# Performance work log

Hardware: AMD Instinct MI355X
Metric: run time of the kernel (lower is better)

Reference implementation:

```python
import jax, jax.numpy as jnp
import numpy as np

N_NODES = 100000
N_EDGES = 1600000
IN_DIM = 128      # 1 (degree) + 127 (raw feat)
HID = 128
N_GRAPHS = 100


def setup_inputs() -> dict:
    key = jax.random.key(0)
    ks = jax.random.split(key, 16)
    feat = jax.random.normal(ks[0], (N_NODES, IN_DIM - 1), dtype=jnp.float32)
    src = jax.random.randint(ks[1], (N_EDGES,), 0, N_NODES, dtype=jnp.int32)
    dst = jax.random.randint(ks[2], (N_EDGES,), 0, N_NODES, dtype=jnp.int32)
    graph_ids = jnp.sort(jax.random.randint(ks[3], (N_NODES,), 0, N_GRAPHS, dtype=jnp.int32))
    s = 1.0 / np.sqrt(IN_DIM)
    W0 = jax.random.uniform(ks[4], (HID, IN_DIM), jnp.float32, -s, s)
    b0 = jax.random.uniform(ks[5], (HID,), jnp.float32, -s, s)
    s = 1.0 / np.sqrt(HID)
    W1 = jax.random.uniform(ks[6], (HID, HID), jnp.float32, -s, s)
    b1 = jax.random.uniform(ks[7], (HID,), jnp.float32, -s, s)
    W2 = jax.random.uniform(ks[8], (HID, HID), jnp.float32, -s, s)
    b2 = jax.random.uniform(ks[9], (HID,), jnp.float32, -s, s)
    Wc1 = jax.random.uniform(ks[10], (HID, HID), jnp.float32, -s, s)
    bc1 = jax.random.uniform(ks[11], (HID,), jnp.float32, -s, s)
    Wc2 = jax.random.uniform(ks[12], (1, HID), jnp.float32, -s, s)
    bc2 = jax.random.uniform(ks[13], (1,), jnp.float32, -s, s)
    return {"feat": feat, "src": src, "dst": dst, "graph_ids": graph_ids,
            "num_graphs": N_GRAPHS,
            "W0": W0, "b0": b0, "W1": W1, "b1": b1, "W2": W2, "b2": b2,
            "Wc1": Wc1, "bc1": bc1, "Wc2": Wc2, "bc2": bc2}


def _gcn_layer(h, src, dst, deg, W, b):
    # mean over in-neighbor messages; zero-in-degree nodes keep old h (DGL reduce never fires)
    n = h.shape[0]
    summed = jax.ops.segment_sum(h[src], dst, num_segments=n)  # [N, d]
    mean = summed / jnp.maximum(deg, 1.0)[:, None]
    agg = jnp.where((deg > 0)[:, None], mean, h)
    return jax.nn.relu(agg @ W.T + b)


def reference(feat, src, dst, graph_ids, num_graphs,
              W0, b0, W1, b1, W2, b2, Wc1, bc1, Wc2, bc2):
    n = feat.shape[0]
    deg = jax.ops.segment_sum(jnp.ones(src.shape[0], jnp.float32), dst, num_segments=n)  # in-degrees
    h = jnp.concatenate([deg[:, None], feat], axis=-1)  # [N, IN_DIM]
    for W, b in ((W0, b0), (W1, b1), (W2, b2)):
        h = _gcn_layer(h, src, dst, deg, W, b)
    # dgl.mean_nodes: per-graph mean of node features
    counts = jax.ops.segment_sum(jnp.ones(n, jnp.float32), graph_ids, num_segments=num_graphs)
    hg = jax.ops.segment_sum(h, graph_ids, num_segments=num_graphs) / jnp.maximum(counts, 1.0)[:, None]
    # faithful: classify1 applied twice, no activation (F.relu was passed as bias flag)
    hg = hg @ Wc1.T + bc1
    hg = hg @ Wc1.T + bc1
    hg = hg @ Wc2.T + bc2
    return hg  # [num_graphs, 1]
```

## Files before the change

### kernel.cpp

```cpp
#include <hip/hip_runtime.h>
#include <hip/hip_bf16.h>

#define HID 128
#define NRAW 127
#define BSH 8
#define BNODES 256


typedef __attribute__((ext_vector_type(8))) short short8;
typedef __attribute__((ext_vector_type(4))) float floatx4;
typedef __attribute__((ext_vector_type(2))) float floatx2;

__device__ inline unsigned pack_bf2(float x, float y) {
    unsigned bx = __float_as_uint(x);
    unsigned by = __float_as_uint(y);
    bx += 0x7fffu + ((bx >> 16) & 1u);
    by += 0x7fffu + ((by >> 16) & 1u);
    return (bx >> 16) | (by & 0xffff0000u);
}
__device__ inline float bf_lo(unsigned u) { return __uint_as_float(u << 16); }
__device__ inline float bf_hi(unsigned u) { return __uint_as_float(u & 0xffff0000u); }


__global__ void init_kernel(const float* __restrict__ W0, const float* __restrict__ W1,
                            const float* __restrict__ W2, const float* __restrict__ Wc1,
                            unsigned* __restrict__ O0, unsigned* __restrict__ O1,
                            unsigned* __restrict__ O2, float* __restrict__ Wc1p,
                            int* __restrict__ gbucket, float* __restrict__ hg,
                            float* __restrict__ counts, int G) {
    int id = blockIdx.x * blockDim.x + threadIdx.x;
    if (id < 512) gbucket[id] = 0;
    if (id < G * HID) hg[id] = 0.f;
    if (id < G) counts[id] = 0.f;
    if (id < 16384) {
        int t = id >> 7, p = id & 127;
        Wc1p[id] = Wc1[t * 128 + ((p & 7) * 16 + (p >> 3))];
    }
    if (id < 3 * 8192) {
        int sel = id >> 13, l = id & 8191;
        const float* W = sel == 0 ? W0 : (sel == 1 ? W1 : W2);
        unsigned* O = sel == 0 ? O0 : (sel == 1 ? O1 : O2);
        int o = l >> 6, pp = (l & 63) * 2;
        int k0 = (pp & 7) * 16 + (pp >> 3);
        int k1 = ((pp + 1) & 7) * 16 + ((pp + 1) >> 3);
        O[l] = pack_bf2(W[o * 128 + k0], W[o * 128 + k1]);
    }
}


__global__ __launch_bounds__(256) void bucket_count_kernel(const int* __restrict__ dst,
                                                           int* __restrict__ gbucket,
                                                           int E, int NB) {
    __shared__ int hist[512];
    int t = threadIdx.x;
    for (int b = t; b < NB; b += 256) hist[b] = 0;
    __syncthreads();
    int base = blockIdx.x * 4096;
    #pragma unroll
    for (int j = 0; j < 16; ++j) {
        int e = base + j * 256 + t;
        if (e < E) atomicAdd(&hist[dst[e] >> BSH], 1);
    }
    __syncthreads();
    for (int b = t; b < NB; b += 256) {
        int v = hist[b];
        if (v) atomicAdd(&gbucket[b], v);
    }
}

__global__ void bucket_scan_kernel(const int* __restrict__ gbucket, int* __restrict__ bstart,
                                   int* __restrict__ gcur, int NB, int E) {
    __shared__ int sm[512];
    int t = threadIdx.x;
    int v = (t < NB) ? gbucket[t] : 0;
    sm[t] = v;
    __syncthreads();
    for (int off = 1; off < 512; off <<= 1) {
        int add = (t >= off) ? sm[t - off] : 0;
        __syncthreads();
        sm[t] += add;
        __syncthreads();
    }
    if (t < NB) {
        int ex = sm[t] - v;
        bstart[t] = ex;
        gcur[t] = ex;
    }
    if (t == 0) bstart[NB] = E;
}

__global__ __launch_bounds__(256) void bucket_scatter_kernel(const int* __restrict__ src,
                                                             const int* __restrict__ dst,
                                                             int* __restrict__ gcur,
                                                             uint2* __restrict__ staging,
                                                             int E, int NB) {
    __shared__ int hist[512];
    __shared__ int base[512];
    int t = threadIdx.x;
    for (int b = t; b < NB; b += 256) hist[b] = 0;
    __syncthreads();
    int s[16], d[16], r[16];
    int e0 = blockIdx.x * 4096;
    #pragma unroll
    for (int j = 0; j < 16; ++j) {
        int e = e0 + j * 256 + t;
        if (e < E) {
            s[j] = src[e];
            d[j] = dst[e];
            r[j] = atomicAdd(&hist[d[j] >> BSH], 1);
        } else d[j] = -1;
    }
    __syncthreads();
    for (int b = t; b < NB; b += 256) {
        int v = hist[b];
        base[b] = v ? atomicAdd(&gcur[b], v) : 0;
    }
    __syncthreads();
    #pragma unroll
    for (int j = 0; j < 16; ++j) {
        if (d[j] >= 0) {
            int b = d[j] >> BSH;
            staging[base[b] + r[j]] = make_uint2((unsigned)s[j], (unsigned)d[j]);
        }
    }
}

__global__ __launch_bounds__(256) void csr_build_kernel(const uint2* __restrict__ staging,
                                                        const int* __restrict__ bstart,
                                                        int* __restrict__ rp, int* __restrict__ csr,
                                                        float* __restrict__ degf,
                                                        int N, int E, int NB) {
    __shared__ int hist[256];
    __shared__ int sm[256];
    __shared__ int excl[256];
    __shared__ int cnt[256];
    int t = threadIdx.x;
    int b = blockIdx.x;
    int nbase = b << BSH;
    int s0 = bstart[b], e1 = bstart[b + 1];
    hist[t] = 0;
    __syncthreads();
    for (int i = s0 + t; i < e1; i += 256) {
        uint2 p = staging[i];
        atomicAdd(&hist[p.y & (BNODES - 1)], 1);
    }
    __syncthreads();
    int h = hist[t];
    sm[t] = h;
    __syncthreads();
    for (int off = 1; off < 256; off <<= 1) {
        int add = (t >= off) ? sm[t - off] : 0;
        __syncthreads();
        sm[t] += add;
        __syncthreads();
    }
    excl[t] = sm[t] - h;
    cnt[t] = 0;
    int n = nbase + t;
    if (n < N) {
        rp[n] = s0 + (sm[t] - h);
        degf[n] = (float)h;
    }
    if (b == NB - 1 && t == 0) rp[N] = E;
    __syncthreads();
    for (int i = s0 + t; i < e1; i += 256) {
        uint2 p = staging[i];
        int dl = p.y & (BNODES - 1);
        int pos = s0 + excl[dl] + atomicAdd(&cnt[dl], 1);
        csr[pos] = (int)p.x;
    }
}


__global__ void build_h0_kernel(const float* __restrict__ feat,
                                unsigned* __restrict__ h8, int N) {
    int id = blockIdx.x * blockDim.x + threadIdx.x;
    if (id >= N * 32) return;
    int n = id >> 5, c = id & 31;
    const float* fr = feat + (size_t)n * NRAW;
    int base = c >> 1, hb = (c & 1) * 4;
    float f[4];
    #pragma unroll
    for (int j = 0; j < 4; ++j) {
        int l = (hb + j) * 16 + base;
        f[j] = (l == 0) ? 0.f : fr[l - 1];
    }
    unsigned w = __builtin_amdgcn_cvt_pk_fp8_f32(f[0], f[1], 0, false);
    w = __builtin_amdgcn_cvt_pk_fp8_f32(f[2], f[3], w, true);
    h8[id] = w;
}


__global__ __launch_bounds__(256) void gcn_fused_kernel(const unsigned* __restrict__ h8,
                                                        unsigned* __restrict__ out8,
                                                        unsigned* __restrict__ outb,
                                                        const unsigned* __restrict__ Wb,
                                                        const float* __restrict__ bias,
                                                        const int* __restrict__ rp,
                                                        const int* __restrict__ csr,
                                                        const float* __restrict__ degf, int N) {
    __shared__ unsigned Al[16 * 64];
    __shared__ unsigned Cs[16 * 64];
    int t = threadIdx.x;
    int col = t & 15;
    int g = t >> 4;
    int n0 = blockIdx.x * 16;
    int i = n0 + g;
    const uint2* h2 = (const uint2*)h8;

    if (i < N) {
        int start = rp[i], end = rp[i + 1];
        int deg = end - start;
        uint4 r;
        if (deg == 0) {
            uint2 v = h2[(size_t)i * 16 + col];
            floatx2 l0 = __builtin_amdgcn_cvt_pk_f32_fp8(v.x, false);
            floatx2 h0 = __builtin_amdgcn_cvt_pk_f32_fp8(v.x, true);
            floatx2 l1 = __builtin_amdgcn_cvt_pk_f32_fp8(v.y, false);
            floatx2 h1 = __builtin_amdgcn_cvt_pk_f32_fp8(v.y, true);
            r.x = pack_bf2(l0[0], l0[1]);
            r.y = pack_bf2(h0[0], h0[1]);
            r.z = pack_bf2(l1[0], l1[1]);
            r.w = pack_bf2(h1[0], h1[1]);
        } else {
            floatx2 a0 = {0.f, 0.f}, a1 = {0.f, 0.f}, a2 = {0.f, 0.f}, a3 = {0.f, 0.f};
            float dsum = 0.f;
            int p = start;
            for (; p + 4 <= end; p += 4) {
                int i0 = csr[p];
                int i1 = csr[p + 1];
                int i2 = csr[p + 2];
                int i3 = csr[p + 3];
                uint2 v0 = h2[(size_t)i0 * 16 + col];
                uint2 v1 = h2[(size_t)i1 * 16 + col];
                uint2 v2 = h2[(size_t)i2 * 16 + col];
                uint2 v3 = h2[(size_t)i3 * 16 + col];
                if (degf && col == 0) dsum += degf[i0] + degf[i1] + degf[i2] + degf[i3];
                a0 += __builtin_amdgcn_cvt_pk_f32_fp8(v0.x, false);
                a1 += __builtin_amdgcn_cvt_pk_f32_fp8(v0.x, true);
                a2 += __builtin_amdgcn_cvt_pk_f32_fp8(v0.y, false);
                a3 += __builtin_amdgcn_cvt_pk_f32_fp8(v0.y, true);
                a0 += __builtin_amdgcn_cvt_pk_f32_fp8(v1.x, false);
                a1 += __builtin_amdgcn_cvt_pk_f32_fp8(v1.x, true);
                a2 += __builtin_amdgcn_cvt_pk_f32_fp8(v1.y, false);
                a3 += __builtin_amdgcn_cvt_pk_f32_fp8(v1.y, true);
                a0 += __builtin_amdgcn_cvt_pk_f32_fp8(v2.x, false);
                a1 += __builtin_amdgcn_cvt_pk_f32_fp8(v2.x, true);
                a2 += __builtin_amdgcn_cvt_pk_f32_fp8(v2.y, false);
                a3 += __builtin_amdgcn_cvt_pk_f32_fp8(v2.y, true);
                a0 += __builtin_amdgcn_cvt_pk_f32_fp8(v3.x, false);
                a1 += __builtin_amdgcn_cvt_pk_f32_fp8(v3.x, true);
                a2 += __builtin_amdgcn_cvt_pk_f32_fp8(v3.y, false);
                a3 += __builtin_amdgcn_cvt_pk_f32_fp8(v3.y, true);
            }
            for (; p < end; ++p) {
                int i0 = csr[p];
                uint2 v0 = h2[(size_t)i0 * 16 + col];
                if (degf && col == 0) dsum += degf[i0];
                a0 += __builtin_amdgcn_cvt_pk_f32_fp8(v0.x, false);
                a1 += __builtin_amdgcn_cvt_pk_f32_fp8(v0.x, true);
                a2 += __builtin_amdgcn_cvt_pk_f32_fp8(v0.y, false);
                a3 += __builtin_amdgcn_cvt_pk_f32_fp8(v0.y, true);
            }
            if (degf && col == 0) a0[0] = dsum;
            float inv = 1.f / (float)deg;
            r.x = pack_bf2(a0[0] * inv, a0[1] * inv);
            r.y = pack_bf2(a1[0] * inv, a1[1] * inv);
            r.z = pack_bf2(a2[0] * inv, a2[1] * inv);
            r.w = pack_bf2(a3[0] * inv, a3[1] * inv);
        }
        *(uint4*)&Al[(g * 16 + col) * 4] = r;
    }
    __syncthreads();

    int wv = t >> 6, lane = t & 63;
    int m = lane & 15, q = lane >> 4;
    floatx4 acc0 = (floatx4)(0.f), acc1 = (floatx4)(0.f);
    #pragma unroll
    for (int kt = 0; kt < 4; ++kt) {
        short8 af = *(const short8*)&Al[m * 64 + (kt * 4 + q) * 4];
        short8 b0 = *(const short8*)&Wb[((2 * wv) * 16 + m) * 64 + kt * 16 + q * 4];
        short8 b1 = *(const short8*)&Wb[((2 * wv + 1) * 16 + m) * 64 + kt * 16 + q * 4];
        acc0 = __builtin_amdgcn_mfma_f32_16x16x32_bf16(af, b0, acc0, 0, 0, 0);
        acc1 = __builtin_amdgcn_mfma_f32_16x16x32_bf16(af, b1, acc1, 0, 0, 0);
    }
    float bv0 = bias[(2 * wv) * 16 + m];
    float bv1 = bias[(2 * wv + 1) * 16 + m];
    #pragma unroll
    for (int r4 = 0; r4 < 4; ++r4) {
        int row = q * 4 + r4;
        float v0 = fmaxf(acc0[r4] + bv0, 0.f);
        float v1 = fmaxf(acc1[r4] + bv1, 0.f);
        if (out8) {
            unsigned pk = __builtin_amdgcn_cvt_pk_fp8_f32(v0, v1, 0, false);
            *(unsigned short*)((char*)Cs + row * 128 + m * 8 + 2 * wv) = (unsigned short)pk;
        } else {
            Cs[row * 64 + m * 4 + wv] = pack_bf2(v0, v1);
        }
    }
    __syncthreads();

    {
        int row = t >> 4, c = t & 15;
        int n = n0 + row;
        if (n < N) {
            if (out8)
                ((uint2*)out8)[(size_t)n * 16 + c] =
                    *(const uint2*)((const char*)Cs + row * 128 + c * 8);
            else
                ((uint4*)outb)[(size_t)n * 16 + c] = *(const uint4*)&Cs[row * 64 + c * 4];
        }
    }
}


__global__ __launch_bounds__(256) void pool_kernel(const unsigned* __restrict__ h,
                                                   const int* __restrict__ gid,
                                                   float* __restrict__ hg,
                                                   float* __restrict__ counts, int N) {
    int c = threadIdx.x & 63;
    int q = threadIdx.x >> 6;
    int n0 = blockIdx.x * 64;
    int nend = min(n0 + 64, N);
    float ax = 0.f, ay = 0.f, cnt = 0.f;
    int cur = -1;
    for (int n = n0 + q; n < nend; n += 4) {
        int g = gid[n];
        if (g != cur) {
            if (cur >= 0) {
                atomicAdd(&hg[cur * HID + 2 * c], ax);
                atomicAdd(&hg[cur * HID + 2 * c + 1], ay);
                if (c == 0) atomicAdd(&counts[cur], cnt);
            }
            ax = ay = cnt = 0.f;
            cur = g;
        }
        unsigned v = h[(size_t)n * 64 + c];
        ax += bf_lo(v); ay += bf_hi(v);
        cnt += 1.f;
    }
    if (cur >= 0) {
        atomicAdd(&hg[cur * HID + 2 * c], ax);
        atomicAdd(&hg[cur * HID + 2 * c + 1], ay);
        if (c == 0) atomicAdd(&counts[cur], cnt);
    }
}


__global__ __launch_bounds__(128) void cls_fused_kernel(const float* __restrict__ hg,
                                                        const float* __restrict__ counts,
                                                        const float* __restrict__ Wc1p,
                                                        const float* __restrict__ Wc1,
                                                        const float* __restrict__ bc1,
                                                        const float* __restrict__ Wc2,
                                                        const float* __restrict__ bc2,
                                                        float* __restrict__ out, int G) {
    __shared__ float x[128];
    __shared__ float y[128];
    __shared__ float red[128];
    int g = blockIdx.x, t = threadIdx.x;
    float inv = 1.f / fmaxf(counts[g], 1.f);
    x[t] = hg[g * HID + t] * inv;
    __syncthreads();
    const float4* wp4 = (const float4*)(Wc1p + t * HID);
    float s = 0.f;
    #pragma unroll
    for (int k4 = 0; k4 < 32; ++k4) {
        float4 w = wp4[k4];
        s += x[k4 * 4] * w.x + x[k4 * 4 + 1] * w.y + x[k4 * 4 + 2] * w.z + x[k4 * 4 + 3] * w.w;
    }
    y[t] = s + bc1[t];
    __syncthreads();
    const float4* w4 = (const float4*)(Wc1 + t * HID);
    float s2 = 0.f;
    #pragma unroll
    for (int k4 = 0; k4 < 32; ++k4) {
        float4 w = w4[k4];
        s2 += y[k4 * 4] * w.x + y[k4 * 4 + 1] * w.y + y[k4 * 4 + 2] * w.z + y[k4 * 4 + 3] * w.w;
    }
    red[t] = (s2 + bc1[t]) * Wc2[t];
    __syncthreads();
    if (t < 64) {
        float r = red[t] + red[t + 64];
        #pragma unroll
        for (int off = 32; off > 0; off >>= 1) r += __shfl_down(r, off);
        if (t == 0) out[g] = r + bc2[0];
    }
}


extern "C" void kernel_launch(void* const* d_in, const int* in_sizes, int n_in,
                              void* d_out, int out_size, void* d_ws, size_t ws_size,
                              hipStream_t stream) {
    const float* feat = (const float*)d_in[0];
    const int* src    = (const int*)d_in[1];
    const int* dst    = (const int*)d_in[2];
    const int* gid    = (const int*)d_in[3];
    const float* W0  = (const float*)d_in[5];
    const float* b0  = (const float*)d_in[6];
    const float* W1  = (const float*)d_in[7];
    const float* b1  = (const float*)d_in[8];
    const float* W2  = (const float*)d_in[9];
    const float* b2  = (const float*)d_in[10];
    const float* Wc1 = (const float*)d_in[11];
    const float* bc1 = (const float*)d_in[12];
    const float* Wc2 = (const float*)d_in[13];
    const float* bc2 = (const float*)d_in[14];

    const int N = in_sizes[3];
    const int E = in_sizes[1];
    const int G = out_size;
    const int NB = (N + BNODES - 1) >> BSH;

    char* ws = (char*)d_ws;
    size_t off = 0;
    auto alloc = [&](size_t bytes) { void* p = ws + off; off += (bytes + 255) & ~size_t(255); return p; };
    unsigned* h8a    = (unsigned*)alloc((size_t)N * 32 * 4);
    unsigned* h8b    = (unsigned*)alloc((size_t)N * 32 * 4);
    unsigned* hB     = (unsigned*)alloc((size_t)N * 64 * 4);
    float* degf      = (float*)alloc((size_t)N * 4);
    uint2* staging   = (uint2*)alloc((size_t)E * 8);
    int* csr         = (int*)alloc((size_t)E * 4);
    int* rp          = (int*)alloc((size_t)(N + 1) * 4);
    int* gbucket     = (int*)alloc(512 * 4);
    int* bstart      = (int*)alloc(513 * 4);
    int* gcur        = (int*)alloc(512 * 4);
    unsigned* Wb0    = (unsigned*)alloc(8192 * 4);
    unsigned* Wb1    = (unsigned*)alloc(8192 * 4);
    unsigned* Wb2    = (unsigned*)alloc(8192 * 4);
    float* Wc1p      = (float*)alloc(16384 * 4);
    float* hg        = (float*)alloc((size_t)G * HID * 4);
    float* counts    = (float*)alloc((size_t)G * 4);

    init_kernel<<<96, 256, 0, stream>>>(W0, W1, W2, Wc1, Wb0, Wb1, Wb2, Wc1p,
                                        gbucket, hg, counts, G);

    int gE = (E + 4095) / 4096;
    bucket_count_kernel<<<gE, 256, 0, stream>>>(dst, gbucket, E, NB);
    bucket_scan_kernel<<<1, 512, 0, stream>>>(gbucket, bstart, gcur, NB, E);
    bucket_scatter_kernel<<<gE, 256, 0, stream>>>(src, dst, gcur, staging, E, NB);
    csr_build_kernel<<<NB, 256, 0, stream>>>(staging, bstart, rp, csr, degf, N, E, NB);

    build_h0_kernel<<<(N * 32 + 255) / 256, 256, 0, stream>>>(feat, h8a, N);

    int layer_grid = (N + 15) / 16;
    gcn_fused_kernel<<<layer_grid, 256, 0, stream>>>(h8a, h8b, nullptr, Wb0, b0, rp, csr, degf, N);
    gcn_fused_kernel<<<layer_grid, 256, 0, stream>>>(h8b, h8a, nullptr, Wb1, b1, rp, csr, nullptr, N);
    gcn_fused_kernel<<<layer_grid, 256, 0, stream>>>(h8a, nullptr, hB, Wb2, b2, rp, csr, nullptr, N);

    pool_kernel<<<(N + 63) / 64, 256, 0, stream>>>(hB, gid, hg, counts, N);

    cls_fused_kernel<<<G, 128, 0, stream>>>(hg, counts, Wc1p, Wc1, bc1, Wc2, bc2,
                                            (float*)d_out, G);
}
```

Before: 379.9 us.

## Stage block CSR indices in LDS, pack staging edges, swizzle A tile

The GCN aggregation kernel now loads each 16-node block's contiguous CSR neighbor indices cooperatively into shared memory in windows, then gathers from LDS with an 8-way unrolled loop and 32-bit offset arithmetic. Edge staging is packed into one 32-bit word (src<<8 | local dst), which halves staging traffic in scatter and CSR build; this relies on src fitting in 24 bits. The A-tile LDS layout is XOR-swizzled to reduce bank conflicts on the MFMA operand reads. Blocks with many edges now loop over several windows with extra barriers.

```diff
diff --git a/kernel.cpp b/kernel.cpp
--- a/kernel.cpp
+++ b/kernel.cpp
@@ -5,6 +5,7 @@
 #define NRAW 127
 #define BSH 8
 #define BNODES 256
+#define EW 1536
 
 
 typedef __attribute__((ext_vector_type(8))) short short8;
@@ -92,7 +93,7 @@
 __global__ __launch_bounds__(256) void bucket_scatter_kernel(const int* __restrict__ src,
                                                              const int* __restrict__ dst,
                                                              int* __restrict__ gcur,
-                                                             uint2* __restrict__ staging,
+                                                             unsigned* __restrict__ staging,
                                                              int E, int NB) {
     __shared__ int hist[512];
     __shared__ int base[512];
@@ -120,12 +121,12 @@
     for (int j = 0; j < 16; ++j) {
         if (d[j] >= 0) {
             int b = d[j] >> BSH;
-            staging[base[b] + r[j]] = make_uint2((unsigned)s[j], (unsigned)d[j]);
-        }
-    }
-}
-
-__global__ __launch_bounds__(256) void csr_build_kernel(const uint2* __restrict__ staging,
+            staging[base[b] + r[j]] = ((unsigned)s[j] << 8) | ((unsigned)d[j] & 255u);
+        }
+    }
+}
+
+__global__ __launch_bounds__(256) void csr_build_kernel(const unsigned* __restrict__ staging,
                                                         const int* __restrict__ bstart,
                                                         int* __restrict__ rp, int* __restrict__ csr,
                                                         float* __restrict__ degf,
@@ -141,8 +142,8 @@
     hist[t] = 0;
     __syncthreads();
     for (int i = s0 + t; i < e1; i += 256) {
-        uint2 p = staging[i];
-        atomicAdd(&hist[p.y & (BNODES - 1)], 1);
+        unsigned p = staging[i];
+        atomicAdd(&hist[p & (BNODES - 1)], 1);
     }
     __syncthreads();
     int h = hist[t];
@@ -164,10 +165,10 @@
     if (b == NB - 1 && t == 0) rp[N] = E;
     __syncthreads();
     for (int i = s0 + t; i < e1; i += 256) {
-        uint2 p = staging[i];
-        int dl = p.y & (BNODES - 1);
+        unsigned p = staging[i];
+        int dl = p & (BNODES - 1);
         int pos = s0 + excl[dl] + atomicAdd(&cnt[dl], 1);
-        csr[pos] = (int)p.x;
+        csr[pos] = (int)(p >> 8);
     }
 }
 
@@ -201,19 +202,70 @@
                                                         const float* __restrict__ degf, int N) {
     __shared__ unsigned Al[16 * 64];
     __shared__ unsigned Cs[16 * 64];
+    __shared__ int sIdx[EW];
     int t = threadIdx.x;
     int col = t & 15;
     int g = t >> 4;
     int n0 = blockIdx.x * 16;
     int i = n0 + g;
-    const uint2* h2 = (const uint2*)h8;
+    const char* hbase = (const char*)h8;
+    unsigned cOff = (unsigned)col * 8u;
+
+    int start = 0, end = 0;
+    if (i < N) { start = rp[i]; end = rp[i + 1]; }
+    int deg = end - start;
+    int nEnd = min(n0 + 16, N);
+    int s0 = rp[n0];
+    int e1 = rp[nEnd];
+
+    floatx2 a0 = {0.f, 0.f}, a1 = {0.f, 0.f}, a2 = {0.f, 0.f}, a3 = {0.f, 0.f};
+    float dsum = 0.f;
+
+    #define GATH(ii) (*(const uint2*)(hbase + (((unsigned)(ii) << 7) + cOff)))
+    #define ACC(vv) do { \
+        a0 += __builtin_amdgcn_cvt_pk_f32_fp8((vv).x, false); \
+        a1 += __builtin_amdgcn_cvt_pk_f32_fp8((vv).x, true);  \
+        a2 += __builtin_amdgcn_cvt_pk_f32_fp8((vv).y, false); \
+        a3 += __builtin_amdgcn_cvt_pk_f32_fp8((vv).y, true);  \
+    } while (0)
+
+    for (int w0 = s0; w0 < e1; w0 += EW) {
+        if (w0 > s0) __syncthreads();
+        int wcnt = min(EW, e1 - w0);
+        for (int j = t; j < wcnt; j += 256) sIdx[j] = csr[w0 + j];
+        __syncthreads();
+        int p = max(start, w0) - w0;
+        int pe = min(end, w0 + wcnt) - w0;
+        for (; p + 8 <= pe; p += 8) {
+            int i0 = sIdx[p],     i1 = sIdx[p + 1], i2 = sIdx[p + 2], i3 = sIdx[p + 3];
+            int i4 = sIdx[p + 4], i5 = sIdx[p + 5], i6 = sIdx[p + 6], i7 = sIdx[p + 7];
+            uint2 v0 = GATH(i0), v1 = GATH(i1), v2 = GATH(i2), v3 = GATH(i3);
+            uint2 v4 = GATH(i4), v5 = GATH(i5), v6 = GATH(i6), v7 = GATH(i7);
+            if (degf && col == 0)
+                dsum += degf[i0] + degf[i1] + degf[i2] + degf[i3]
+                      + degf[i4] + degf[i5] + degf[i6] + degf[i7];
+            ACC(v0); ACC(v1); ACC(v2); ACC(v3);
+            ACC(v4); ACC(v5); ACC(v6); ACC(v7);
+        }
+        for (; p + 4 <= pe; p += 4) {
+            int i0 = sIdx[p], i1 = sIdx[p + 1], i2 = sIdx[p + 2], i3 = sIdx[p + 3];
+            uint2 v0 = GATH(i0), v1 = GATH(i1), v2 = GATH(i2), v3 = GATH(i3);
+            if (degf && col == 0)
+                dsum += degf[i0] + degf[i1] + degf[i2] + degf[i3];
+            ACC(v0); ACC(v1); ACC(v2); ACC(v3);
+        }
+        for (; p < pe; ++p) {
+            int i0 = sIdx[p];
+            uint2 v0 = GATH(i0);
+            if (degf && col == 0) dsum += degf[i0];
+            ACC(v0);
+        }
+    }
 
     if (i < N) {
-        int start = rp[i], end = rp[i + 1];
-        int deg = end - start;
         uint4 r;
         if (deg == 0) {
-            uint2 v = h2[(size_t)i * 16 + col];
+            uint2 v = GATH(i);
             floatx2 l0 = __builtin_amdgcn_cvt_pk_f32_fp8(v.x, false);
             floatx2 h0 = __builtin_amdgcn_cvt_pk_f32_fp8(v.x, true);
             floatx2 l1 = __builtin_amdgcn_cvt_pk_f32_fp8(v.y, false);
@@ -223,45 +275,6 @@
             r.z = pack_bf2(l1[0], l1[1]);
             r.w = pack_bf2(h1[0], h1[1]);
         } else {
-            floatx2 a0 = {0.f, 0.f}, a1 = {0.f, 0.f}, a2 = {0.f, 0.f}, a3 = {0.f, 0.f};
-            float dsum = 0.f;
-            int p = start;
-            for (; p + 4 <= end; p += 4) {
-                int i0 = csr[p];
-                int i1 = csr[p + 1];
-                int i2 = csr[p + 2];
-                int i3 = csr[p + 3];
-                uint2 v0 = h2[(size_t)i0 * 16 + col];
-                uint2 v1 = h2[(size_t)i1 * 16 + col];
-                uint2 v2 = h2[(size_t)i2 * 16 + col];
-                uint2 v3 = h2[(size_t)i3 * 16 + col];
-                if (degf && col == 0) dsum += degf[i0] + degf[i1] + degf[i2] + degf[i3];
-                a0 += __builtin_amdgcn_cvt_pk_f32_fp8(v0.x, false);
-                a1 += __builtin_amdgcn_cvt_pk_f32_fp8(v0.x, true);
-                a2 += __builtin_amdgcn_cvt_pk_f32_fp8(v0.y, false);
-                a3 += __builtin_amdgcn_cvt_pk_f32_fp8(v0.y, true);
-                a0 += __builtin_amdgcn_cvt_pk_f32_fp8(v1.x, false);
-                a1 += __builtin_amdgcn_cvt_pk_f32_fp8(v1.x, true);
-                a2 += __builtin_amdgcn_cvt_pk_f32_fp8(v1.y, false);
-                a3 += __builtin_amdgcn_cvt_pk_f32_fp8(v1.y, true);
-                a0 += __builtin_amdgcn_cvt_pk_f32_fp8(v2.x, false);
-                a1 += __builtin_amdgcn_cvt_pk_f32_fp8(v2.x, true);
-                a2 += __builtin_amdgcn_cvt_pk_f32_fp8(v2.y, false);
-                a3 += __builtin_amdgcn_cvt_pk_f32_fp8(v2.y, true);
-                a0 += __builtin_amdgcn_cvt_pk_f32_fp8(v3.x, false);
-                a1 += __builtin_amdgcn_cvt_pk_f32_fp8(v3.x, true);
-                a2 += __builtin_amdgcn_cvt_pk_f32_fp8(v3.y, false);
-                a3 += __builtin_amdgcn_cvt_pk_f32_fp8(v3.y, true);
-            }
-            for (; p < end; ++p) {
-                int i0 = csr[p];
-                uint2 v0 = h2[(size_t)i0 * 16 + col];
-                if (degf && col == 0) dsum += degf[i0];
-                a0 += __builtin_amdgcn_cvt_pk_f32_fp8(v0.x, false);
-                a1 += __builtin_amdgcn_cvt_pk_f32_fp8(v0.x, true);
-                a2 += __builtin_amdgcn_cvt_pk_f32_fp8(v0.y, false);
-                a3 += __builtin_amdgcn_cvt_pk_f32_fp8(v0.y, true);
-            }
             if (degf && col == 0) a0[0] = dsum;
             float inv = 1.f / (float)deg;
             r.x = pack_bf2(a0[0] * inv, a0[1] * inv);
@@ -269,7 +282,7 @@
             r.z = pack_bf2(a2[0] * inv, a2[1] * inv);
             r.w = pack_bf2(a3[0] * inv, a3[1] * inv);
         }
-        *(uint4*)&Al[(g * 16 + col) * 4] = r;
+        *(uint4*)&Al[(g * 16 + (col ^ (g & 7))) * 4] = r;
     }
     __syncthreads();
 
@@ -278,7 +291,7 @@
     floatx4 acc0 = (floatx4)(0.f), acc1 = (floatx4)(0.f);
     #pragma unroll
     for (int kt = 0; kt < 4; ++kt) {
-        short8 af = *(const short8*)&Al[m * 64 + (kt * 4 + q) * 4];
+        short8 af = *(const short8*)&Al[(m * 16 + ((kt * 4 + q) ^ (m & 7))) * 4];
         short8 b0 = *(const short8*)&Wb[((2 * wv) * 16 + m) * 64 + kt * 16 + q * 4];
         short8 b1 = *(const short8*)&Wb[((2 * wv + 1) * 16 + m) * 64 + kt * 16 + q * 4];
         acc0 = __builtin_amdgcn_mfma_f32_16x16x32_bf16(af, b0, acc0, 0, 0, 0);
@@ -311,6 +324,8 @@
                 ((uint4*)outb)[(size_t)n * 16 + c] = *(const uint4*)&Cs[row * 64 + c * 4];
         }
     }
+    #undef GATH
+    #undef ACC
 }
 
 
@@ -419,7 +434,7 @@
     unsigned* h8b    = (unsigned*)alloc((size_t)N * 32 * 4);
     unsigned* hB     = (unsigned*)alloc((size_t)N * 64 * 4);
     float* degf      = (float*)alloc((size_t)N * 4);
-    uint2* staging   = (uint2*)alloc((size_t)E * 8);
+    unsigned* staging = (unsigned*)alloc((size_t)E * 4);
     int* csr         = (int*)alloc((size_t)E * 4);
     int* rp          = (int*)alloc((size_t)(N + 1) * 4);
     int* gbucket     = (int*)alloc(512 * 4);
```

After: 361.5 us. 1.05x faster.
